# Kernel tuning notes

Measured on AMD Instinct MI355X. Metric: run time of the kernel, lower is better.

The kernel has to match this reference:

```python
import jax, jax.numpy as jnp
import numpy as np

B, P, C, F = 16, 1000, 91, 1024      # images, proposals/img, classes (incl bg), box-head dim
H, W = 800, 800                      # image shape (all images same size)
SCORE_THRESH = 0.05
NMS_THRESH = 0.5
DETS = 100                           # detections_per_img
MIN_SIZE = 1e-2
BBOX_XFORM_CLIP = float(np.log(1000.0 / 16.0))
OFF = float(max(H, W) + 2)           # class offset unit for batched (class-aware) NMS


def setup_inputs() -> dict:
    key = jax.random.key(0)
    k1, k2, k3, k4 = jax.random.split(key, 4)
    box_features = jax.random.normal(k1, (B * P, F), jnp.float32)
    Wc = jax.random.normal(k2, (F, C), jnp.float32) * 0.02
    bc = jnp.zeros((C,), jnp.float32)
    Wb = jax.random.normal(k3, (F, C * 4), jnp.float32) * 0.02
    bb = jnp.zeros((C * 4,), jnp.float32)
    u = jax.random.uniform(k4, (B, P, 4), jnp.float32)
    x1 = u[..., 0] * (W * 0.8)
    y1 = u[..., 1] * (H * 0.8)
    x2 = x1 + 16.0 + u[..., 2] * (W * 0.2)
    y2 = y1 + 16.0 + u[..., 3] * (H * 0.2)
    proposals = jnp.stack([x1, y1, x2, y2], axis=-1)
    return dict(box_features=box_features, Wc=Wc, bc=bc, Wb=Wb, bb=bb,
                proposals=proposals)


def _decode_and_clip(regs, props):
    # regs: [N, C, 4] deltas; props: [N, 4] xyxy. bbox_reg_weights = (1,1,1,1).
    w = props[:, 2] - props[:, 0]
    h = props[:, 3] - props[:, 1]
    cx = props[:, 0] + 0.5 * w
    cy = props[:, 1] + 0.5 * h
    dx, dy = regs[..., 0], regs[..., 1]
    dw = jnp.minimum(regs[..., 2], BBOX_XFORM_CLIP)
    dh = jnp.minimum(regs[..., 3], BBOX_XFORM_CLIP)
    pcx = dx * w[:, None] + cx[:, None]
    pcy = dy * h[:, None] + cy[:, None]
    pw = jnp.exp(dw) * w[:, None]
    ph = jnp.exp(dh) * h[:, None]
    x1 = jnp.clip(pcx - 0.5 * pw, 0.0, float(W))
    y1 = jnp.clip(pcy - 0.5 * ph, 0.0, float(H))
    x2 = jnp.clip(pcx + 0.5 * pw, 0.0, float(W))
    y2 = jnp.clip(pcy + 0.5 * ph, 0.0, float(H))
    return jnp.stack([x1, y1, x2, y2], axis=-1)  # [N, C, 4]


def _iou_one_vs_all(box, boxes):
    ix1 = jnp.maximum(box[0], boxes[:, 0])
    iy1 = jnp.maximum(box[1], boxes[:, 1])
    ix2 = jnp.minimum(box[2], boxes[:, 2])
    iy2 = jnp.minimum(box[3], boxes[:, 3])
    inter = jnp.clip(ix2 - ix1, 0.0) * jnp.clip(iy2 - iy1, 0.0)
    a1 = (box[2] - box[0]) * (box[3] - box[1])
    a2 = (boxes[:, 2] - boxes[:, 0]) * (boxes[:, 3] - boxes[:, 1])
    return inter / (a1 + a2 - inter + 1e-9)


def _greedy_nms(boxes, scores):
    # boxes: [M,4] (class-offset), scores: [M] (-inf = filtered out).
    # Returns selected indices [DETS] and scores [DETS] (0 where no valid pick).
    def body(i, st):
        sc, sel, ss = st
        j = jnp.argmax(sc)
        s = sc[j]
        iou = _iou_one_vs_all(boxes[j], boxes)
        sc = jnp.where(iou > NMS_THRESH, -jnp.inf, sc)  # suppresses j itself too
        valid = s > 0.0
        sel = sel.at[i].set(jnp.where(valid, j.astype(jnp.int32), 0))
        ss = ss.at[i].set(jnp.where(valid, s, 0.0))
        return sc, sel, ss
    init = (scores, jnp.zeros((DETS,), jnp.int32), jnp.zeros((DETS,), jnp.float32))
    _, sel, ss = jax.lax.fori_loop(0, DETS, body, init)
    return sel, ss


def reference(box_features, Wc, bc, Wb, bb, proposals):
    # Box predictor (FastRCNNPredictor-style linear heads).
    class_logits = box_features @ Wc + bc                  # [B*P, C]
    box_regression = (box_features @ Wb + bb).reshape(-1, C, 4)
    # Decode per-class boxes against proposals, clip to image.
    pred = _decode_and_clip(box_regression, proposals.reshape(-1, 4))  # [B*P, C, 4]
    scores = jax.nn.softmax(class_logits, axis=-1)         # [B*P, C]
    # Drop background class 0; flatten (proposal, class) per image.
    M = P * (C - 1)
    boxes_all = pred[:, 1:, :].reshape(B, M, 4)
    scores_all = scores[:, 1:].reshape(B, M)
    labels_all = jnp.tile(jnp.arange(1, C, dtype=jnp.int32), P)  # [M]
    # Score threshold + remove tiny boxes (mask instead of dynamic filter).
    bw = boxes_all[..., 2] - boxes_all[..., 0]
    bh = boxes_all[..., 3] - boxes_all[..., 1]
    keep = (scores_all > SCORE_THRESH) & (bw >= MIN_SIZE) & (bh >= MIN_SIZE)
    scores_m = jnp.where(keep, scores_all, -jnp.inf)
    # Class-aware batched NMS via per-class coordinate offsets.
    boxes_off = boxes_all + (labels_all.astype(jnp.float32) * OFF)[None, :, None]
    sel, det_scores = jax.vmap(_greedy_nms)(boxes_off, scores_m)   # [B,DETS]
    det_boxes = jnp.take_along_axis(boxes_all, sel[..., None], axis=1)  # [B,DETS,4]
    det_labels = labels_all[sel]                                        # [B,DETS]
    valid = det_scores > 0.0
    det_boxes = det_boxes * valid[..., None]
    det_labels = jnp.where(valid, det_labels, 0)
    return det_boxes, det_scores, det_labels
```

## Files before the change

### kernel.cpp

```cpp
#include <hip/hip_runtime.h>
#include <hip/hip_bf16.h>
#include <math.h>

typedef unsigned long long ull;

#define BB_ 16
#define PP_ 1000
#define CC_ 91
#define FF_ 1024
#define DETS_ 100
#define CAP_ 2048
#define CAND_MAX (BB_ * CAP_)
#define SURV_CAP 2048
#define CLS_CAP 256
#define IMG_W 800.0f
#define IMG_H 800.0f
#define OFF_ 802.0f
#define SCORE_TH 0.05f
#define PRE_TH 0.047f
#define NMS_TH 0.5f
#define MIN_SZ 0.01f
#define BBOX_CLIP_D 4.135166556742356

__global__ __launch_bounds__(256) void wb_transpose(
    const float* __restrict__ Wb, float* __restrict__ Wbt)
{
    const int idx = blockIdx.x * 256 + threadIdx.x;
    if (idx >= CC_ * 4 * FF_) return;
    const int c = idx >> 12;
    const int j = (idx >> 10) & 3;
    const int k = idx & 1023;
    if (c < 1) { Wbt[idx] = 0.f; return; }
    Wbt[idx] = Wb[(size_t)k * (CC_ * 4) + 4 * c + j];
}

__global__ __launch_bounds__(512) void prepass_rows(
    const float* __restrict__ A, const float* __restrict__ Wc,
    const float* __restrict__ bc,
    int* __restrict__ rowlist, int* __restrict__ nrowsp)
{
    __shared__ union __align__(16) SM {
        struct { float Af[2][16][34]; float Bs[2][16][98]; } t;
        float Ssc[32][97];
    } sm;
    __shared__ float comb[256][12];

    const int tid = threadIdx.x;
    const int kg = tid >> 8;
    const int l = tid & 255;
    const int row0 = blockIdx.x * 32;
    const int kbase = kg * 512;
    const int ty2 = (l >> 4) * 2;
    const int tx6 = (l & 15) * 6;

    const int am = l >> 2;
    const int ak = (l & 3) * 4;
    const int bk = l >> 4;
    const int bn = (l & 15) * 6;

    float acc[2][6];
#pragma unroll
    for (int i = 0; i < 2; ++i)
#pragma unroll
        for (int j = 0; j < 6; ++j) acc[i][j] = 0.f;

    float4 avP = make_float4(0.f, 0.f, 0.f, 0.f);
    if (l < 128)
        avP = *reinterpret_cast<const float4*>(
            A + (size_t)(row0 + am) * FF_ + kbase + ak);
    float bvP[6];
#pragma unroll
    for (int jj = 0; jj < 6; ++jj) {
        const int c = bn + jj;
        bvP[jj] = (c < CC_) ? Wc[(size_t)(kbase + bk) * CC_ + c] : 0.f;
    }

    for (int k0 = 0; k0 < 512; k0 += 16) {
        if (l < 128) {
            sm.t.Af[kg][ak + 0][am] = avP.x;
            sm.t.Af[kg][ak + 1][am] = avP.y;
            sm.t.Af[kg][ak + 2][am] = avP.z;
            sm.t.Af[kg][ak + 3][am] = avP.w;
        }
#pragma unroll
        for (int jj = 0; jj < 6; ++jj) sm.t.Bs[kg][bk][bn + jj] = bvP[jj];

        const int kn = k0 + 16;
        if (kn < 512) {
            if (l < 128)
                avP = *reinterpret_cast<const float4*>(
                    A + (size_t)(row0 + am) * FF_ + kbase + kn + ak);
#pragma unroll
            for (int jj = 0; jj < 6; ++jj) {
                const int c = bn + jj;
                bvP[jj] = (c < CC_) ? Wc[(size_t)(kbase + kn + bk) * CC_ + c] : 0.f;
            }
        }
        __syncthreads();

#pragma unroll
        for (int k = 0; k < 16; ++k) {
            const float2 af = *reinterpret_cast<const float2*>(&sm.t.Af[kg][k][ty2]);
            const float2 b01 = *reinterpret_cast<const float2*>(&sm.t.Bs[kg][k][tx6 + 0]);
            const float2 b23 = *reinterpret_cast<const float2*>(&sm.t.Bs[kg][k][tx6 + 2]);
            const float2 b45 = *reinterpret_cast<const float2*>(&sm.t.Bs[kg][k][tx6 + 4]);
            const float a0 = af.x, a1 = af.y;
            acc[0][0] += a0 * b01.x; acc[0][1] += a0 * b01.y;
            acc[0][2] += a0 * b23.x; acc[0][3] += a0 * b23.y;
            acc[0][4] += a0 * b45.x; acc[0][5] += a0 * b45.y;
            acc[1][0] += a1 * b01.x; acc[1][1] += a1 * b01.y;
            acc[1][2] += a1 * b23.x; acc[1][3] += a1 * b23.y;
            acc[1][4] += a1 * b45.x; acc[1][5] += a1 * b45.y;
        }
        __syncthreads();
    }

    if (kg == 1) {
#pragma unroll
        for (int i = 0; i < 2; ++i)
#pragma unroll
            for (int j = 0; j < 6; ++j) comb[l][i * 6 + j] = acc[i][j];
    }
    __syncthreads();
    if (kg == 0) {
#pragma unroll
        for (int i = 0; i < 2; ++i)
#pragma unroll
            for (int j = 0; j < 6; ++j) {
                const int c = tx6 + j;
                if (c < CC_)
                    sm.Ssc[ty2 + i][c] = acc[i][j] + comb[l][i * 6 + j] + bc[c];
            }
    }
    __syncthreads();

    if (tid < 32) {
        float m_all = sm.Ssc[tid][0];
        float m_fg = -INFINITY;
        for (int c = 1; c < CC_; ++c) {
            const float lv = sm.Ssc[tid][c];
            m_all = fmaxf(m_all, lv);
            m_fg = fmaxf(m_fg, lv);
        }
        float denom = 0.f;
        for (int c = 0; c < CC_; ++c) denom += expf(sm.Ssc[tid][c] - m_all);
        const float maxsc = expf(m_fg - m_all) / denom;
        if (maxsc > PRE_TH) {
            const int pos = atomicAdd(nrowsp, 1);
            rowlist[pos] = row0 + tid;
        }
    }
}

__global__ __launch_bounds__(512) void logits_fp64_rows(
    const float* __restrict__ A, const float* __restrict__ Wc,
    const float* __restrict__ bc,
    const int* __restrict__ rowlist, const int* __restrict__ nrowsp,
    float* __restrict__ cs, int* __restrict__ clab,
    int* __restrict__ corig, int* __restrict__ cpidx,
    int* __restrict__ cnt)
{
    const int nr = *nrowsp;
    const int row0 = blockIdx.x * 8;
    if (row0 >= nr) return;

    __shared__ __align__(16) float Af[2][16][12];
    __shared__ __align__(16) float Bs[2][16][98];
    __shared__ __align__(16) double dcomb[256][3];
    __shared__ float Ssc[8][97];

    const int tid = threadIdx.x;
    const int kg = tid >> 8;
    const int l = tid & 255;
    const int kbase = kg * 512;
    const int r = l >> 5;
    const int c0 = (l & 31) * 3;

    const int aslot = l >> 2;
    const int akq = (l & 3) * 4;
    const float* Arow = nullptr;
    if (l < 32) {
        const int ridx = min(row0 + aslot, nr - 1);
        Arow = A + (size_t)rowlist[ridx] * FF_ + kbase;
    }
    const int bk = l >> 4;
    const int bn = (l & 15) * 6;

    double acc[3] = {0.0, 0.0, 0.0};

    float4 avP = make_float4(0.f, 0.f, 0.f, 0.f);
    if (l < 32) avP = *reinterpret_cast<const float4*>(Arow + akq);
    float bvP[6];
#pragma unroll
    for (int jj = 0; jj < 6; ++jj) {
        const int c = bn + jj;
        bvP[jj] = (c < CC_) ? Wc[(size_t)(kbase + bk) * CC_ + c] : 0.f;
    }

    for (int k0 = 0; k0 < 512; k0 += 16) {
        if (l < 32) {
            Af[kg][akq + 0][aslot] = avP.x;
            Af[kg][akq + 1][aslot] = avP.y;
            Af[kg][akq + 2][aslot] = avP.z;
            Af[kg][akq + 3][aslot] = avP.w;
        }
#pragma unroll
        for (int jj = 0; jj < 6; ++jj) Bs[kg][bk][bn + jj] = bvP[jj];

        const int kn = k0 + 16;
        if (kn < 512) {
            if (l < 32)
                avP = *reinterpret_cast<const float4*>(Arow + kn + akq);
#pragma unroll
            for (int jj = 0; jj < 6; ++jj) {
                const int c = bn + jj;
                bvP[jj] = (c < CC_) ? Wc[(size_t)(kbase + kn + bk) * CC_ + c] : 0.f;
            }
        }
        __syncthreads();

#pragma unroll
        for (int k = 0; k < 16; ++k) {
            const double a0 = (double)Af[kg][k][r];
            const double b0 = (double)Bs[kg][k][c0 + 0];
            const double b1 = (double)Bs[kg][k][c0 + 1];
            const double b2 = (double)Bs[kg][k][c0 + 2];
            acc[0] += a0 * b0;
            acc[1] += a0 * b1;
            acc[2] += a0 * b2;
        }
        __syncthreads();
    }

    if (kg == 1) {
#pragma unroll
        for (int j = 0; j < 3; ++j) dcomb[l][j] = acc[j];
    }
    __syncthreads();
    if (kg == 0) {
#pragma unroll
        for (int j = 0; j < 3; ++j) {
            const int c = c0 + j;
            if (c < CC_) {
                const double v = acc[j] + dcomb[l][j];
                Ssc[r][c] = __fadd_rn((float)v, bc[c]);
            }
        }
    }
    __syncthreads();

    {
        const int w = tid >> 6;
        if (w < 8 && row0 + w < nr) {
            const int lane = tid & 63;
            const int p = rowlist[row0 + w];
            const int b = p / PP_;
            const int pi = p - b * PP_;

            const float l1 = Ssc[w][lane];
            const float l2 = (lane < CC_ - 64) ? Ssc[w][lane + 64] : -INFINITY;
            float m = fmaxf(l1, l2);
#pragma unroll
            for (int off = 32; off > 0; off >>= 1)
                m = fmaxf(m, __shfl_xor(m, off));

            double d = exp((double)l1 - (double)m);
            if (lane < CC_ - 64) d += exp((double)l2 - (double)m);
#pragma unroll
            for (int off = 1; off < 64; off <<= 1)
                d += __shfl_xor(d, off);

#pragma unroll
            for (int q = 0; q < 2; ++q) {
                const int c = lane + q * 64;
                if (c >= 1 && c < CC_) {
                    const double sd = exp((double)Ssc[w][c] - (double)m) / d;
                    const float score = (float)sd;
                    if (score > SCORE_TH) {
                        const int pos = atomicAdd(&cnt[b], 1);
                        if (pos < CAP_) {
                            const int g = b * CAP_ + pos;
                            cs[g] = score;
                            clab[g] = c;
                            corig[g] = pi * (CC_ - 1) + (c - 1);
                            cpidx[g] = p;
                        }
                    }
                }
            }
        }
    }
}

template<bool USE_T>
__global__ __launch_bounds__(256) void decode_cand_k(
    const float* __restrict__ A, const float* __restrict__ Wb,
    const float* __restrict__ Wbt,
    const float* __restrict__ bb, const float* __restrict__ props,
    const int* __restrict__ cnt, const int* __restrict__ clab,
    const int* __restrict__ cpidx,
    float* __restrict__ cs, float* __restrict__ cx1, float* __restrict__ cy1,
    float* __restrict__ cx2, float* __restrict__ cy2)
{
    const int wid = (blockIdx.x * 256 + threadIdx.x) >> 6;
    const int lane = threadIdx.x & 63;
    const int b = wid / CAP_;
    const int pos = wid - b * CAP_;
    if (b >= BB_) return;
    const int n = min(cnt[b], CAP_);
    if (pos >= n) return;

    const int g = b * CAP_ + pos;
    const int p = cpidx[g];
    const int c = clab[g];

    const float* fr = A + (size_t)p * FF_;

    double a0 = 0.0, a1 = 0.0, a2 = 0.0, a3 = 0.0;
    if (USE_T) {
        const float* w0 = Wbt + (size_t)c * 4096;
        for (int k = lane; k < FF_; k += 64) {
            const double f = (double)fr[k];
            a0 += f * (double)w0[k];
            a1 += f * (double)w0[1024 + k];
            a2 += f * (double)w0[2048 + k];
            a3 += f * (double)w0[3072 + k];
        }
    } else {
        const float* wb0 = Wb + 4 * c;
        for (int k = lane; k < FF_; k += 64) {
            const double f = (double)fr[k];
            const float4 wv = *reinterpret_cast<const float4*>(wb0 + (size_t)k * (CC_ * 4));
            a0 += f * (double)wv.x; a1 += f * (double)wv.y;
            a2 += f * (double)wv.z; a3 += f * (double)wv.w;
        }
    }
#pragma unroll
    for (int off = 32; off > 0; off >>= 1) {
        a0 += __shfl_xor(a0, off);
        a1 += __shfl_xor(a1, off);
        a2 += __shfl_xor(a2, off);
        a3 += __shfl_xor(a3, off);
    }

    if (lane == 0) {
        const float dx = __fadd_rn((float)a0, bb[4 * c + 0]);
        const float dy = __fadd_rn((float)a1, bb[4 * c + 1]);
        const float clipf = (float)BBOX_CLIP_D;
        const float dw = fminf(__fadd_rn((float)a2, bb[4 * c + 2]), clipf);
        const float dh = fminf(__fadd_rn((float)a3, bb[4 * c + 3]), clipf);

        const float px1 = props[(size_t)p * 4 + 0];
        const float py1 = props[(size_t)p * 4 + 1];
        const float px2 = props[(size_t)p * 4 + 2];
        const float py2 = props[(size_t)p * 4 + 3];
        const float w = __fsub_rn(px2, px1);
        const float h = __fsub_rn(py2, py1);
        const float cx = __fadd_rn(px1, __fmul_rn(0.5f, w));
        const float cy = __fadd_rn(py1, __fmul_rn(0.5f, h));

        const float pcx = __fadd_rn(__fmul_rn(dx, w), cx);
        const float pcy = __fadd_rn(__fmul_rn(dy, h), cy);
        const float ew = (float)exp((double)dw);
        const float eh = (float)exp((double)dh);
        const float pw = __fmul_rn(ew, w);
        const float ph = __fmul_rn(eh, h);

        const float hw = __fmul_rn(0.5f, pw);
        const float hh = __fmul_rn(0.5f, ph);
        const float bx1 = fminf(fmaxf(__fsub_rn(pcx, hw), 0.f), IMG_W);
        const float by1 = fminf(fmaxf(__fsub_rn(pcy, hh), 0.f), IMG_H);
        const float bx2 = fminf(fmaxf(__fadd_rn(pcx, hw), 0.f), IMG_W);
        const float by2 = fminf(fmaxf(__fadd_rn(pcy, hh), 0.f), IMG_H);

        cx1[g] = bx1; cy1[g] = by1; cx2[g] = bx2; cy2[g] = by2;
        if (!(__fsub_rn(bx2, bx1) >= MIN_SZ && __fsub_rn(by2, by1) >= MIN_SZ)) {
            cs[g] = -INFINITY;
        }
    }
}

__global__ __launch_bounds__(64) void nms_class(
    const float* __restrict__ c_x1, const float* __restrict__ c_y1,
    const float* __restrict__ c_x2, const float* __restrict__ c_y2,
    const float* __restrict__ c_s, const int* __restrict__ c_lab,
    const int* __restrict__ c_orig, const int* __restrict__ cnt,
    ull* __restrict__ skey, float* __restrict__ sx1v, float* __restrict__ sy1v,
    float* __restrict__ sx2v, float* __restrict__ sy2v,
    int* __restrict__ slabv, int* __restrict__ scnt)
{
    const int blk = blockIdx.x;
    const int b = blk / (CC_ - 1);
    const int c = 1 + (blk - b * (CC_ - 1));
    const int lane = threadIdx.x;

    __shared__ ull kk[CLS_CAP];
    __shared__ float x1s[CLS_CAP], y1s[CLS_CAP], x2s[CLS_CAP], y2s[CLS_CAP];

    const int n = min(cnt[b], CAP_);

    int mcnt = 0;
    for (int i0 = 0; i0 < n; i0 += 64) {
        const int i = i0 + lane;
        bool take = false;
        float s = 0.f; int so = 0; int g = 0;
        if (i < n) {
            g = b * CAP_ + i;
            if (c_lab[g] == c) {
                s = c_s[g];
                if (s > 0.f) { take = true; so = c_orig[g]; }
            }
        }
        const ull bal = __ballot(take);
        if (take) {
            const int pos = mcnt + __popcll(bal & ((1ull << lane) - 1ull));
            if (pos < CLS_CAP) {
                kk[pos] = ((ull)__float_as_uint(s) << 32) |
                          (unsigned int)(0x7FFFFFFF - so);
                x1s[pos] = c_x1[g]; y1s[pos] = c_y1[g];
                x2s[pos] = c_x2[g]; y2s[pos] = c_y2[g];
            }
        }
        mcnt += (int)__popcll(bal);
    }
    mcnt = min(mcnt, CLS_CAP);
    if (mcnt == 0) return;
    __syncthreads();

    while (true) {
        ull best = 0ull;
        for (int i = lane; i < mcnt; i += 64) best = (kk[i] > best) ? kk[i] : best;
#pragma unroll
        for (int off = 32; off > 0; off >>= 1) {
            const ull o = __shfl_xor(best, off);
            best = (o > best) ? o : best;
        }
        if (best == 0ull) break;

        int wsl = -1;
        for (int i = lane; i < mcnt; i += 64) if (kk[i] == best) wsl = i;
        const ull bal = __ballot(wsl >= 0);
        const int wlane = (int)__ffsll((long long)bal) - 1;
        wsl = __shfl(wsl, wlane);

        const float wx1 = x1s[wsl], wy1 = y1s[wsl];
        const float wx2 = x2s[wsl], wy2 = y2s[wsl];

        if (lane == 0) {
            const int sp = atomicAdd(&scnt[b], 1);
            if (sp < SURV_CAP) {
                const int sg = b * SURV_CAP + sp;
                skey[sg] = best;
                sx1v[sg] = wx1; sy1v[sg] = wy1;
                sx2v[sg] = wx2; sy2v[sg] = wy2;
                slabv[sg] = c;
            }
        }

        const float off = __fmul_rn((float)c, OFF_);
        const float ax1 = __fadd_rn(wx1, off), ay1 = __fadd_rn(wy1, off);
        const float ax2 = __fadd_rn(wx2, off), ay2 = __fadd_rn(wy2, off);
        const float a1 = __fmul_rn(__fsub_rn(ax2, ax1), __fsub_rn(ay2, ay1));
        for (int i = lane; i < mcnt; i += 64) {
            if (kk[i] == 0ull) continue;
            const float bx1 = __fadd_rn(x1s[i], off), by1 = __fadd_rn(y1s[i], off);
            const float bx2 = __fadd_rn(x2s[i], off), by2 = __fadd_rn(y2s[i], off);
            const float ix1 = fmaxf(ax1, bx1), iy1 = fmaxf(ay1, by1);
            const float ix2 = fminf(ax2, bx2), iy2 = fminf(ay2, by2);
            const float inter = __fmul_rn(fmaxf(__fsub_rn(ix2, ix1), 0.f),
                                          fmaxf(__fsub_rn(iy2, iy1), 0.f));
            const float a2 = __fmul_rn(__fsub_rn(bx2, bx1), __fsub_rn(by2, by1));
            const float den = __fadd_rn(__fsub_rn(__fadd_rn(a1, a2), inter), 1e-9f);
            const float iou = __fdiv_rn(inter, den);
            if (iou > NMS_TH) kk[i] = 0ull;
        }
        __syncthreads();
    }
}

__global__ __launch_bounds__(256) void nms_merge(
    const ull* __restrict__ skey, const float* __restrict__ sx1v,
    const float* __restrict__ sy1v, const float* __restrict__ sx2v,
    const float* __restrict__ sy2v, const int* __restrict__ slabv,
    const int* __restrict__ scnt, float* __restrict__ out)
{
    const int b = blockIdx.x;
    const int t = threadIdx.x;

    __shared__ ull k_[SURV_CAP];
    __shared__ int id_[SURV_CAP];

    const int m = min(scnt[b], SURV_CAP);
    int N2 = 128;
    while (N2 < m) N2 <<= 1;

    for (int i = t; i < N2; i += 256) {
        k_[i] = (i < m) ? skey[b * SURV_CAP + i] : 0ull;
        id_[i] = i;
    }
    __syncthreads();

    for (int ksz = 2; ksz <= N2; ksz <<= 1) {
        for (int j = ksz >> 1; j > 0; j >>= 1) {
            for (int i = t; i < N2; i += 256) {
                const int ixj = i ^ j;
                if (ixj > i) {
                    const ull a = k_[i], cc = k_[ixj];
                    const bool desc = ((i & ksz) == 0);
                    if (desc ? (a < cc) : (a > cc)) {
                        k_[i] = cc; k_[ixj] = a;
                        const int tmp = id_[i]; id_[i] = id_[ixj]; id_[ixj] = tmp;
                    }
                }
            }
            __syncthreads();
        }
    }

    const int boxes_base = 0;
    const int scores_base = BB_ * DETS_ * 4;
    const int labels_base = BB_ * DETS_ * 5;

    for (int r = t; r < DETS_; r += 256) {
        const ull key = (r < N2) ? k_[r] : 0ull;
        float* bo = out + boxes_base + (size_t)(b * DETS_ + r) * 4;
        if (key != 0ull) {
            const int sg = b * SURV_CAP + id_[r];
            bo[0] = sx1v[sg]; bo[1] = sy1v[sg];
            bo[2] = sx2v[sg]; bo[3] = sy2v[sg];
            out[scores_base + b * DETS_ + r] = __uint_as_float((unsigned)(key >> 32));
            out[labels_base + b * DETS_ + r] = (float)slabv[sg];
        } else {
            bo[0] = 0.f; bo[1] = 0.f; bo[2] = 0.f; bo[3] = 0.f;
            out[scores_base + b * DETS_ + r] = 0.f;
            out[labels_base + b * DETS_ + r] = 0.f;
        }
    }
}

extern "C" void kernel_launch(void* const* d_in, const int* in_sizes, int n_in,
                              void* d_out, int out_size, void* d_ws, size_t ws_size,
                              hipStream_t stream)
{
    const float* feat  = (const float*)d_in[0];
    const float* Wc    = (const float*)d_in[1];
    const float* bc    = (const float*)d_in[2];
    const float* Wb    = (const float*)d_in[3];
    const float* bb    = (const float*)d_in[4];
    const float* props = (const float*)d_in[5];
    for (int i = 0; i < n_in; ++i) {
        const float* q = (const float*)d_in[i];
        switch (in_sizes[i]) {
            case 16384000: feat  = q; break;
            case 93184:    Wc    = q; break;
            case 91:       bc    = q; break;
            case 372736:   Wb    = q; break;
            case 364:      bb    = q; break;
            case 64000:    props = q; break;
        }
    }
    float* out = (float*)d_out;

    char* ws = (char*)d_ws;
    int*   cnt    = (int*)ws;
    int*   scnt   = (int*)(ws + 64);
    int*   nrowsp = (int*)(ws + 128);
    float* cs    = (float*)(ws + 256);
    int*   clab  = (int*)(cs + CAND_MAX);
    int*   corig = clab + CAND_MAX;
    int*   cpidx = corig + CAND_MAX;
    float* cx1   = (float*)(cpidx + CAND_MAX);
    float* cy1   = cx1 + CAND_MAX;
    float* cx2   = cy1 + CAND_MAX;
    float* cy2   = cx2 + CAND_MAX;
    ull*   skey  = (ull*)(cy2 + CAND_MAX);
    float* sx1v  = (float*)(skey + (size_t)BB_ * SURV_CAP);
    float* sy1v  = sx1v + (size_t)BB_ * SURV_CAP;
    float* sx2v  = sy1v + (size_t)BB_ * SURV_CAP;
    float* sy2v  = sx2v + (size_t)BB_ * SURV_CAP;
    int*   slabv = (int*)(sy2v + (size_t)BB_ * SURV_CAP);
    int*   rowlist = slabv + (size_t)BB_ * SURV_CAP;
    float* Wbt   = (float*)(rowlist + 16384);

    const size_t need = ((char*)(Wbt + CC_ * 4 * FF_)) - ws;
    const bool useT = (ws_size >= need);

    hipMemsetAsync(ws, 0, 256, stream);

    if (useT)
        wb_transpose<<<(CC_ * 4 * FF_ + 255) / 256, 256, 0, stream>>>(Wb, Wbt);

    prepass_rows<<<BB_ * PP_ / 32, 512, 0, stream>>>(feat, Wc, bc,
        rowlist, nrowsp);

    logits_fp64_rows<<<BB_ * PP_ / 8, 512, 0, stream>>>(feat, Wc, bc,
        rowlist, nrowsp, cs, clab, corig, cpidx, cnt);

    if (useT)
        decode_cand_k<true><<<CAND_MAX / 4, 256, 0, stream>>>(feat, Wb, Wbt,
            bb, props, cnt, clab, cpidx, cs, cx1, cy1, cx2, cy2);
    else
        decode_cand_k<false><<<CAND_MAX / 4, 256, 0, stream>>>(feat, Wb, Wbt,
            bb, props, cnt, clab, cpidx, cs, cx1, cy1, cx2, cy2);

    nms_class<<<BB_ * (CC_ - 1), 64, 0, stream>>>(
        cx1, cy1, cx2, cy2, cs, clab, corig, cnt,
        skey, sx1v, sy1v, sx2v, sy2v, slabv, scnt);

    nms_merge<<<BB_, 256, 0, stream>>>(
        skey, sx1v, sy1v, sx2v, sy2v, slabv, scnt, out);
}
```

Baseline: 288.5 us.

## Fuse candidate box decode into fp64 logits kernel and widen K tile

```diff
diff --git a/kernel.cpp b/kernel.cpp
--- a/kernel.cpp
+++ b/kernel.cpp
@@ -13,6 +13,7 @@
 #define CAND_MAX (BB_ * CAP_)
 #define SURV_CAP 2048
 #define CLS_CAP 256
+#define BLK_CAND 720
 #define IMG_W 800.0f
 #define IMG_H 800.0f
 #define OFF_ 802.0f
@@ -152,22 +153,29 @@
     }
 }
 
+template<bool USE_T>
 __global__ __launch_bounds__(512) void logits_fp64_rows(
     const float* __restrict__ A, const float* __restrict__ Wc,
     const float* __restrict__ bc,
+    const float* __restrict__ Wb, const float* __restrict__ Wbt,
+    const float* __restrict__ bb, const float* __restrict__ props,
     const int* __restrict__ rowlist, const int* __restrict__ nrowsp,
     float* __restrict__ cs, int* __restrict__ clab,
     int* __restrict__ corig, int* __restrict__ cpidx,
-    int* __restrict__ cnt)
+    int* __restrict__ cnt,
+    float* __restrict__ cx1, float* __restrict__ cy1,
+    float* __restrict__ cx2, float* __restrict__ cy2)
 {
     const int nr = *nrowsp;
     const int row0 = blockIdx.x * 8;
     if (row0 >= nr) return;
 
-    __shared__ __align__(16) float Af[2][16][12];
-    __shared__ __align__(16) float Bs[2][16][98];
-    __shared__ __align__(16) double dcomb[256][3];
-    __shared__ float Ssc[8][97];
+    __shared__ union __align__(16) SM {
+        struct { double Ad[2][32][8]; double Bd[2][32][96]; } t;
+        struct { double dcomb[256][3]; float Ssc[8][97];
+                 int cp[BLK_CAND]; int cc[BLK_CAND]; int cg[BLK_CAND]; } u;
+    } sm;
+    __shared__ int ncand;
 
     const int tid = threadIdx.x;
     const int kg = tid >> 8;
@@ -176,43 +184,46 @@
     const int r = l >> 5;
     const int c0 = (l & 31) * 3;
 
-    const int aslot = l >> 2;
-    const int akq = (l & 3) * 4;
+    if (tid == 0) ncand = 0;
+
+    const int aslot = l >> 3;
+    const int akq = (l & 7) * 4;
     const float* Arow = nullptr;
-    if (l < 32) {
+    if (l < 64) {
         const int ridx = min(row0 + aslot, nr - 1);
         Arow = A + (size_t)rowlist[ridx] * FF_ + kbase;
     }
-    const int bk = l >> 4;
-    const int bn = (l & 15) * 6;
+    const int bk = l >> 3;
+    const int bn = (l & 7) * 12;
 
     double acc[3] = {0.0, 0.0, 0.0};
 
     float4 avP = make_float4(0.f, 0.f, 0.f, 0.f);
-    if (l < 32) avP = *reinterpret_cast<const float4*>(Arow + akq);
-    float bvP[6];
-#pragma unroll
-    for (int jj = 0; jj < 6; ++jj) {
+    if (l < 64) avP = *reinterpret_cast<const float4*>(Arow + akq);
+    float bvP[12];
+#pragma unroll
+    for (int jj = 0; jj < 12; ++jj) {
         const int c = bn + jj;
         bvP[jj] = (c < CC_) ? Wc[(size_t)(kbase + bk) * CC_ + c] : 0.f;
     }
 
-    for (int k0 = 0; k0 < 512; k0 += 16) {
-        if (l < 32) {
-            Af[kg][akq + 0][aslot] = avP.x;
-            Af[kg][akq + 1][aslot] = avP.y;
-            Af[kg][akq + 2][aslot] = avP.z;
-            Af[kg][akq + 3][aslot] = avP.w;
-        }
-#pragma unroll
-        for (int jj = 0; jj < 6; ++jj) Bs[kg][bk][bn + jj] = bvP[jj];
-
-        const int kn = k0 + 16;
+    for (int k0 = 0; k0 < 512; k0 += 32) {
+        if (l < 64) {
+            sm.t.Ad[kg][akq + 0][aslot] = (double)avP.x;
+            sm.t.Ad[kg][akq + 1][aslot] = (double)avP.y;
+            sm.t.Ad[kg][akq + 2][aslot] = (double)avP.z;
+            sm.t.Ad[kg][akq + 3][aslot] = (double)avP.w;
+        }
+#pragma unroll
+        for (int jj = 0; jj < 12; ++jj)
+            sm.t.Bd[kg][bk][bn + jj] = (double)bvP[jj];
+
+        const int kn = k0 + 32;
         if (kn < 512) {
-            if (l < 32)
+            if (l < 64)
                 avP = *reinterpret_cast<const float4*>(Arow + kn + akq);
 #pragma unroll
-            for (int jj = 0; jj < 6; ++jj) {
+            for (int jj = 0; jj < 12; ++jj) {
                 const int c = bn + jj;
                 bvP[jj] = (c < CC_) ? Wc[(size_t)(kbase + kn + bk) * CC_ + c] : 0.f;
             }
@@ -220,11 +231,11 @@
         __syncthreads();
 
 #pragma unroll
-        for (int k = 0; k < 16; ++k) {
-            const double a0 = (double)Af[kg][k][r];
-            const double b0 = (double)Bs[kg][k][c0 + 0];
-            const double b1 = (double)Bs[kg][k][c0 + 1];
-            const double b2 = (double)Bs[kg][k][c0 + 2];
+        for (int k = 0; k < 32; ++k) {
+            const double a0 = sm.t.Ad[kg][k][r];
+            const double b0 = sm.t.Bd[kg][k][c0 + 0];
+            const double b1 = sm.t.Bd[kg][k][c0 + 1];
+            const double b2 = sm.t.Bd[kg][k][c0 + 2];
             acc[0] += a0 * b0;
             acc[1] += a0 * b1;
             acc[2] += a0 * b2;
@@ -234,7 +245,7 @@
 
     if (kg == 1) {
 #pragma unroll
-        for (int j = 0; j < 3; ++j) dcomb[l][j] = acc[j];
+        for (int j = 0; j < 3; ++j) sm.u.dcomb[l][j] = acc[j];
     }
     __syncthreads();
     if (kg == 0) {
@@ -242,8 +253,8 @@
         for (int j = 0; j < 3; ++j) {
             const int c = c0 + j;
             if (c < CC_) {
-                const double v = acc[j] + dcomb[l][j];
-                Ssc[r][c] = __fadd_rn((float)v, bc[c]);
+                const double v = acc[j] + sm.u.dcomb[l][j];
+                sm.u.Ssc[r][c] = __fadd_rn((float)v, bc[c]);
             }
         }
     }
@@ -251,14 +262,14 @@
 
     {
         const int w = tid >> 6;
+        const int lane = tid & 63;
         if (w < 8 && row0 + w < nr) {
-            const int lane = tid & 63;
             const int p = rowlist[row0 + w];
             const int b = p / PP_;
             const int pi = p - b * PP_;
 
-            const float l1 = Ssc[w][lane];
-            const float l2 = (lane < CC_ - 64) ? Ssc[w][lane + 64] : -INFINITY;
+            const float l1 = sm.u.Ssc[w][lane];
+            const float l2 = (lane < CC_ - 64) ? sm.u.Ssc[w][lane + 64] : -INFINITY;
             float m = fmaxf(l1, l2);
 #pragma unroll
             for (int off = 32; off > 0; off >>= 1)
@@ -274,7 +285,7 @@
             for (int q = 0; q < 2; ++q) {
                 const int c = lane + q * 64;
                 if (c >= 1 && c < CC_) {
-                    const double sd = exp((double)Ssc[w][c] - (double)m) / d;
+                    const double sd = exp((double)sm.u.Ssc[w][c] - (double)m) / d;
                     const float score = (float)sd;
                     if (score > SCORE_TH) {
                         const int pos = atomicAdd(&cnt[b], 1);
@@ -284,98 +295,93 @@
                             clab[g] = c;
                             corig[g] = pi * (CC_ - 1) + (c - 1);
                             cpidx[g] = p;
+                            const int slot = atomicAdd(&ncand, 1);
+                            if (slot < BLK_CAND) {
+                                sm.u.cp[slot] = p;
+                                sm.u.cc[slot] = c;
+                                sm.u.cg[slot] = g;
+                            }
                         }
                     }
                 }
             }
         }
     }
-}
-
-template<bool USE_T>
-__global__ __launch_bounds__(256) void decode_cand_k(
-    const float* __restrict__ A, const float* __restrict__ Wb,
-    const float* __restrict__ Wbt,
-    const float* __restrict__ bb, const float* __restrict__ props,
-    const int* __restrict__ cnt, const int* __restrict__ clab,
-    const int* __restrict__ cpidx,
-    float* __restrict__ cs, float* __restrict__ cx1, float* __restrict__ cy1,
-    float* __restrict__ cx2, float* __restrict__ cy2)
-{
-    const int wid = (blockIdx.x * 256 + threadIdx.x) >> 6;
-    const int lane = threadIdx.x & 63;
-    const int b = wid / CAP_;
-    const int pos = wid - b * CAP_;
-    if (b >= BB_) return;
-    const int n = min(cnt[b], CAP_);
-    if (pos >= n) return;
-
-    const int g = b * CAP_ + pos;
-    const int p = cpidx[g];
-    const int c = clab[g];
-
-    const float* fr = A + (size_t)p * FF_;
-
-    double a0 = 0.0, a1 = 0.0, a2 = 0.0, a3 = 0.0;
-    if (USE_T) {
-        const float* w0 = Wbt + (size_t)c * 4096;
-        for (int k = lane; k < FF_; k += 64) {
-            const double f = (double)fr[k];
-            a0 += f * (double)w0[k];
-            a1 += f * (double)w0[1024 + k];
-            a2 += f * (double)w0[2048 + k];
-            a3 += f * (double)w0[3072 + k];
-        }
-    } else {
-        const float* wb0 = Wb + 4 * c;
-        for (int k = lane; k < FF_; k += 64) {
-            const double f = (double)fr[k];
-            const float4 wv = *reinterpret_cast<const float4*>(wb0 + (size_t)k * (CC_ * 4));
-            a0 += f * (double)wv.x; a1 += f * (double)wv.y;
-            a2 += f * (double)wv.z; a3 += f * (double)wv.w;
-        }
-    }
-#pragma unroll
-    for (int off = 32; off > 0; off >>= 1) {
-        a0 += __shfl_xor(a0, off);
-        a1 += __shfl_xor(a1, off);
-        a2 += __shfl_xor(a2, off);
-        a3 += __shfl_xor(a3, off);
-    }
-
-    if (lane == 0) {
-        const float dx = __fadd_rn((float)a0, bb[4 * c + 0]);
-        const float dy = __fadd_rn((float)a1, bb[4 * c + 1]);
-        const float clipf = (float)BBOX_CLIP_D;
-        const float dw = fminf(__fadd_rn((float)a2, bb[4 * c + 2]), clipf);
-        const float dh = fminf(__fadd_rn((float)a3, bb[4 * c + 3]), clipf);
-
-        const float px1 = props[(size_t)p * 4 + 0];
-        const float py1 = props[(size_t)p * 4 + 1];
-        const float px2 = props[(size_t)p * 4 + 2];
-        const float py2 = props[(size_t)p * 4 + 3];
-        const float w = __fsub_rn(px2, px1);
-        const float h = __fsub_rn(py2, py1);
-        const float cx = __fadd_rn(px1, __fmul_rn(0.5f, w));
-        const float cy = __fadd_rn(py1, __fmul_rn(0.5f, h));
-
-        const float pcx = __fadd_rn(__fmul_rn(dx, w), cx);
-        const float pcy = __fadd_rn(__fmul_rn(dy, h), cy);
-        const float ew = (float)exp((double)dw);
-        const float eh = (float)exp((double)dh);
-        const float pw = __fmul_rn(ew, w);
-        const float ph = __fmul_rn(eh, h);
-
-        const float hw = __fmul_rn(0.5f, pw);
-        const float hh = __fmul_rn(0.5f, ph);
-        const float bx1 = fminf(fmaxf(__fsub_rn(pcx, hw), 0.f), IMG_W);
-        const float by1 = fminf(fmaxf(__fsub_rn(pcy, hh), 0.f), IMG_H);
-        const float bx2 = fminf(fmaxf(__fadd_rn(pcx, hw), 0.f), IMG_W);
-        const float by2 = fminf(fmaxf(__fadd_rn(pcy, hh), 0.f), IMG_H);
-
-        cx1[g] = bx1; cy1[g] = by1; cx2[g] = bx2; cy2[g] = by2;
-        if (!(__fsub_rn(bx2, bx1) >= MIN_SZ && __fsub_rn(by2, by1) >= MIN_SZ)) {
-            cs[g] = -INFINITY;
+    __syncthreads();
+
+    {
+        const int w = tid >> 6;
+        const int lane = tid & 63;
+        const int nc = min(ncand, BLK_CAND);
+        for (int ci = w; ci < nc; ci += 8) {
+            const int p = sm.u.cp[ci];
+            const int c = sm.u.cc[ci];
+            const int g = sm.u.cg[ci];
+
+            const float* fr = A + (size_t)p * FF_;
+            double a0 = 0.0, a1 = 0.0, a2 = 0.0, a3 = 0.0;
+            if (USE_T) {
+                const float* w0 = Wbt + (size_t)c * 4096;
+                for (int k = lane; k < FF_; k += 64) {
+                    const double f = (double)fr[k];
+                    a0 += f * (double)w0[k];
+                    a1 += f * (double)w0[1024 + k];
+                    a2 += f * (double)w0[2048 + k];
+                    a3 += f * (double)w0[3072 + k];
+                }
+            } else {
+                const float* wb0 = Wb + 4 * c;
+                for (int k = lane; k < FF_; k += 64) {
+                    const double f = (double)fr[k];
+                    const float4 wv = *reinterpret_cast<const float4*>(
+                        wb0 + (size_t)k * (CC_ * 4));
+                    a0 += f * (double)wv.x; a1 += f * (double)wv.y;
+                    a2 += f * (double)wv.z; a3 += f * (double)wv.w;
+                }
+            }
+#pragma unroll
+            for (int off = 32; off > 0; off >>= 1) {
+                a0 += __shfl_xor(a0, off);
+                a1 += __shfl_xor(a1, off);
+                a2 += __shfl_xor(a2, off);
+                a3 += __shfl_xor(a3, off);
+            }
+
+            if (lane == 0) {
+                const float dx = __fadd_rn((float)a0, bb[4 * c + 0]);
+                const float dy = __fadd_rn((float)a1, bb[4 * c + 1]);
+                const float clipf = (float)BBOX_CLIP_D;
+                const float dw = fminf(__fadd_rn((float)a2, bb[4 * c + 2]), clipf);
+                const float dh = fminf(__fadd_rn((float)a3, bb[4 * c + 3]), clipf);
+
+                const float px1 = props[(size_t)p * 4 + 0];
+                const float py1 = props[(size_t)p * 4 + 1];
+                const float px2 = props[(size_t)p * 4 + 2];
+                const float py2 = props[(size_t)p * 4 + 3];
+                const float wq = __fsub_rn(px2, px1);
+                const float hq = __fsub_rn(py2, py1);
+                const float cxq = __fadd_rn(px1, __fmul_rn(0.5f, wq));
+                const float cyq = __fadd_rn(py1, __fmul_rn(0.5f, hq));
+
+                const float pcx = __fadd_rn(__fmul_rn(dx, wq), cxq);
+                const float pcy = __fadd_rn(__fmul_rn(dy, hq), cyq);
+                const float ew = (float)exp((double)dw);
+                const float eh = (float)exp((double)dh);
+                const float pw = __fmul_rn(ew, wq);
+                const float ph = __fmul_rn(eh, hq);
+
+                const float hw = __fmul_rn(0.5f, pw);
+                const float hh = __fmul_rn(0.5f, ph);
+                const float bx1 = fminf(fmaxf(__fsub_rn(pcx, hw), 0.f), IMG_W);
+                const float by1 = fminf(fmaxf(__fsub_rn(pcy, hh), 0.f), IMG_H);
+                const float bx2 = fminf(fmaxf(__fadd_rn(pcx, hw), 0.f), IMG_W);
+                const float by2 = fminf(fmaxf(__fadd_rn(pcy, hh), 0.f), IMG_H);
+
+                cx1[g] = bx1; cy1[g] = by1; cx2[g] = bx2; cy2[g] = by2;
+                if (!(__fsub_rn(bx2, bx1) >= MIN_SZ && __fsub_rn(by2, by1) >= MIN_SZ)) {
+                    cs[g] = -INFINITY;
+                }
+            }
         }
     }
 }
@@ -593,15 +599,14 @@
     prepass_rows<<<BB_ * PP_ / 32, 512, 0, stream>>>(feat, Wc, bc,
         rowlist, nrowsp);
 
-    logits_fp64_rows<<<BB_ * PP_ / 8, 512, 0, stream>>>(feat, Wc, bc,
-        rowlist, nrowsp, cs, clab, corig, cpidx, cnt);
-
     if (useT)
-        decode_cand_k<true><<<CAND_MAX / 4, 256, 0, stream>>>(feat, Wb, Wbt,
-            bb, props, cnt, clab, cpidx, cs, cx1, cy1, cx2, cy2);
+        logits_fp64_rows<true><<<BB_ * PP_ / 8, 512, 0, stream>>>(
+            feat, Wc, bc, Wb, Wbt, bb, props, rowlist, nrowsp,
+            cs, clab, corig, cpidx, cnt, cx1, cy1, cx2, cy2);
     else
-        decode_cand_k<false><<<CAND_MAX / 4, 256, 0, stream>>>(feat, Wb, Wbt,
-            bb, props, cnt, clab, cpidx, cs, cx1, cy1, cx2, cy2);
+        logits_fp64_rows<false><<<BB_ * PP_ / 8, 512, 0, stream>>>(
+            feat, Wc, bc, Wb, Wbt, bb, props, rowlist, nrowsp,
+            cs, clab, corig, cpidx, cnt, cx1, cy1, cx2, cy2);
 
     nms_class<<<BB_ * (CC_ - 1), 64, 0, stream>>>(
         cx1, cy1, cx2, cy2, cs, clab, corig, cnt,
```

After: 333.0 us. 1.15x slower.
